# Performance work log

Measured on AMD Instinct MI355X. Metric: run time of the kernel, lower is better.

The kernel has to match this reference:

```python
import jax, jax.numpy as jnp
import numpy as np

D_MODEL = 1024
N_HEAD = 16
B, S = 4, 1024


def _linear(x, W, b):
    # torch nn.Linear: y = x @ W.T + b, W: [out, in]
    return jnp.einsum('bsd,ed->bse', x, W) + b


def _split(x):
    b, s, d = x.shape
    return x.reshape(b, s, N_HEAD, d // N_HEAD).transpose(0, 2, 1, 3)  # [b,h,s,dh]


def _concat(x):
    b, h, s, dh = x.shape
    return x.transpose(0, 2, 1, 3).reshape(b, s, h * dh)


def _attention(q, k, v):
    dh = q.shape[-1]
    scale = 1.0 / np.float32(np.sqrt(dh))
    scores = jnp.einsum('bhqd,bhkd->bhqk', q, k) * scale
    probs = jax.nn.softmax(scores, axis=-1)
    return jnp.einsum('bhqk,bhkd->bhqd', probs, v)


def setup_inputs() -> dict:
    key = jax.random.key(0)
    ks = jax.random.split(key, 20)
    sc = 1.0 / np.float32(np.sqrt(D_MODEL))
    inp = {
        'q': jax.random.normal(ks[0], (B, S, D_MODEL), jnp.float32),
        'k': jax.random.normal(ks[1], (B, S, D_MODEL), jnp.float32),
        'v': jax.random.normal(ks[2], (B, S, D_MODEL), jnp.float32),
    }
    names = ['Wq', 'Wk', 'Wv', 'Wq2', 'Wk2', 'Wv2', 'Wc', 'Wc2']
    for i, n in enumerate(names):
        inp[n] = jax.random.normal(ks[3 + i], (D_MODEL, D_MODEL), jnp.float32) * sc
        inp['b' + n[1:]] = jnp.zeros((D_MODEL,), jnp.float32)
    return inp


def reference(q, k, v, Wq, bq, Wk, bk, Wv, bv, Wq2, bq2, Wk2, bk2, Wv2, bv2, Wc, bc, Wc2, bc2):
    # path 1 projections
    q1 = _linear(q, Wq, bq)
    k1 = _linear(k, Wk, bk)
    v1 = _linear(v, Wv, bv)
    # path 2 projections (note cross-wiring: q2 from k, k2/v2 from q)
    q2 = _linear(k, Wq2, bq2)
    k2 = _linear(q, Wk2, bk2)
    v2 = _linear(q, Wv2, bv2)

    out1 = _attention(_split(q1), _split(k1), _split(v1))
    out2 = _attention(_split(q2), _split(k2), _split(v2))

    out1 = _linear(_concat(out1), Wc, bc)
    out2 = _linear(_concat(out2), Wc2, bc2)
    return out1, out2
```

## Files before the change

### kernel.cpp

```cpp
#include <hip/hip_runtime.h>
#include <hip/hip_bf16.h>

#define B_ 4
#define S_ 1024
#define D_ 1024
#define H_ 16
#define M_ 4096

typedef unsigned short u16;
typedef __attribute__((ext_vector_type(4))) float f32x4;
typedef __attribute__((ext_vector_type(16))) float f32x16;
typedef __attribute__((ext_vector_type(8))) short short8;
typedef __attribute__((ext_vector_type(4))) u16 u16x4;

__device__ inline u16 f2bf(float f) {
  return __builtin_bit_cast(u16, __float2bfloat16(f));
}

__device__ inline short8 ldfrag(const u16* p) {
  return *reinterpret_cast<const short8*>(p);
}

__device__ inline void gload_lds16(const void* g, void* l) {
  __builtin_amdgcn_global_load_lds((const __attribute__((address_space(1))) void*)g,
                                   (__attribute__((address_space(3))) void*)l,
                                   16, 0, 0);
}

__device__ inline int sigma_s(int s) {
  return (s & ~12) | ((s & 4) << 1) | ((s & 8) >> 1);
}

struct GArgs {
  const void* A[6];
  const void* W[6];
  const float* bias[6];
  void* C[6];
  float oscale[6];
  int vtrans[6];
};

struct CvtArgs {
  const float* src[11];
  u16* dst[11];
  int n4[11];
};

__global__ __launch_bounds__(256) void cvt_f32_bf16(CvtArgs a) {
  const int z = blockIdx.y;
  const float4* s = (const float4*)a.src[z];
  u16x4* d = (u16x4*)a.dst[z];
  const int n4 = a.n4[z];
  for (int i = blockIdx.x * blockDim.x + threadIdx.x; i < n4; i += gridDim.x * blockDim.x) {
    float4 v = s[i];
    u16x4 o;
    o[0] = f2bf(v.x); o[1] = f2bf(v.y); o[2] = f2bf(v.z); o[3] = f2bf(v.w);
    d[i] = o;
  }
}

template<typename CT>
__global__ __launch_bounds__(256) void gemm_bt_lds(GArgs args) {
  const int z = blockIdx.z;
  const u16* A = (const u16*)args.A[z];
  const u16* W = (const u16*)args.W[z];
  const float* bias = args.bias[z];
  CT* C = (CT*)args.C[z];
  const float oscale = args.oscale[z];
  const int vtrans = args.vtrans[z];

  __shared__ u16 Al[128 * 64];
  __shared__ u16 Bl[128 * 64];

  const int tid = threadIdx.x;
  const int lane = tid & 63;
  const int w = tid >> 6;
  const int wr = w >> 1, wc = w & 1;
  const int l15 = lane & 15, lhi = lane >> 4;

  const int lin = blockIdx.x + blockIdx.y * 8;
  const int xcd = lin & 7, idx = lin >> 3;
  const int bx = (xcd & 1) * 4 + (idx >> 3);
  const int by = (xcd >> 1) * 8 + (idx & 7);
  const int m0 = by * 128, n0 = bx * 128;

  const int srow = lane >> 3;
  const int scol = (lane & 7) * 8;

  const f32x4 vzero = {0.f, 0.f, 0.f, 0.f};
  f32x4 acc[4][4];
#pragma unroll
  for (int i = 0; i < 4; ++i)
#pragma unroll
    for (int j = 0; j < 4; ++j) acc[i][j] = vzero;

  for (int kt = 0; kt < 1024; kt += 64) {
    __syncthreads();
    const u16* Ag = A + (size_t)m0 * 1024 + kt;
    const u16* Wg = W + (size_t)n0 * 1024 + kt;
#pragma unroll
    for (int j = 0; j < 4; ++j) {
      int rb = w * 32 + j * 8;
      gload_lds16(Ag + (size_t)(rb + srow) * 1024 + scol, &Al[rb * 64]);
      gload_lds16(Wg + (size_t)(rb + srow) * 1024 + scol, &Bl[rb * 64]);
    }
    __syncthreads();

#pragma unroll
    for (int c = 0; c < 2; ++c) {
      short8 af[4], bfr[4];
#pragma unroll
      for (int i = 0; i < 4; ++i) af[i] = ldfrag(&Al[(wr * 64 + i * 16 + l15) * 64 + c * 32 + lhi * 8]);
#pragma unroll
      for (int j = 0; j < 4; ++j) bfr[j] = ldfrag(&Bl[(wc * 64 + j * 16 + l15) * 64 + c * 32 + lhi * 8]);
#pragma unroll
      for (int i = 0; i < 4; ++i)
#pragma unroll
        for (int j = 0; j < 4; ++j)
          acc[i][j] = __builtin_amdgcn_mfma_f32_16x16x32_bf16(af[i], bfr[j], acc[i][j], 0, 0, 0);
    }
  }

#pragma unroll
  for (int i = 0; i < 4; ++i) {
#pragma unroll
    for (int j = 0; j < 4; ++j) {
      int n = n0 + wc * 64 + j * 16 + l15;
      float bsv = bias[n];
      int mb = m0 + wr * 64 + i * 16 + lhi * 4;
      if (vtrans) {
        int h = n >> 6, d = n & 63;
        int b = mb >> 10, s0 = sigma_s(mb & 1023);
        u16x4 ov;
#pragma unroll
        for (int r = 0; r < 4; ++r) ov[r] = f2bf((acc[i][j][r] + bsv) * oscale);
        *reinterpret_cast<u16x4*>((u16*)C + ((size_t)((b * 16 + h) * 64 + d)) * 1024 + s0) = ov;
      } else {
#pragma unroll
        for (int r = 0; r < 4; ++r) {
          float val = (acc[i][j][r] + bsv) * oscale;
          if constexpr (sizeof(CT) == 2) ((u16*)C)[(size_t)(mb + r) * 1024 + n] = f2bf(val);
          else ((float*)C)[(size_t)(mb + r) * 1024 + n] = val;
        }
      }
    }
  }
}

template<typename AT, typename CT>
__global__ __launch_bounds__(256) void gemm_bt_batched(GArgs args) {
  const int z = blockIdx.z;
  const AT* A = (const AT*)args.A[z];
  const float* W = (const float*)args.W[z];
  const float* bias = args.bias[z];
  CT* C = (CT*)args.C[z];
  const float oscale = args.oscale[z];
  const int vtrans = args.vtrans[z];

  __shared__ u16 Al[128][72];
  __shared__ u16 Bl[128][72];

  const int tid = threadIdx.x;
  const int lane = tid & 63;
  const int wid = tid >> 6;
  const int wr = wid >> 1, wc = wid & 1;
  const int m0 = blockIdx.y * 128, n0 = blockIdx.x * 128;
  const int l15 = lane & 15, lhi = lane >> 4;

  const f32x4 vzero = {0.f, 0.f, 0.f, 0.f};
  f32x4 acc[4][4];
#pragma unroll
  for (int i = 0; i < 4; ++i)
#pragma unroll
    for (int j = 0; j < 4; ++j) acc[i][j] = vzero;

  for (int kt = 0; kt < 1024; kt += 64) {
    __syncthreads();
#pragma unroll
    for (int i = 0; i < 8; ++i) {
      int g = tid + i * 256;
      int row = g >> 4, col = (g & 15) * 4;
      u16x4 bv;
      if constexpr (sizeof(AT) == 4) {
        float4 vv = *reinterpret_cast<const float4*>((const float*)A + (size_t)(m0 + row) * 1024 + kt + col);
        bv[0] = f2bf(vv.x); bv[1] = f2bf(vv.y); bv[2] = f2bf(vv.z); bv[3] = f2bf(vv.w);
      } else {
        bv = *reinterpret_cast<const u16x4*>((const u16*)A + (size_t)(m0 + row) * 1024 + kt + col);
      }
      *reinterpret_cast<u16x4*>(&Al[row][col]) = bv;
    }
#pragma unroll
    for (int i = 0; i < 8; ++i) {
      int g = tid + i * 256;
      int row = g >> 4, col = (g & 15) * 4;
      float4 vv = *reinterpret_cast<const float4*>((const float*)W + (size_t)(n0 + row) * 1024 + kt + col);
      u16x4 bv;
      bv[0] = f2bf(vv.x); bv[1] = f2bf(vv.y); bv[2] = f2bf(vv.z); bv[3] = f2bf(vv.w);
      *reinterpret_cast<u16x4*>(&Bl[row][col]) = bv;
    }
    __syncthreads();

#pragma unroll
    for (int c = 0; c < 2; ++c) {
      short8 af[4], bfr[4];
#pragma unroll
      for (int i = 0; i < 4; ++i) af[i] = ldfrag(&Al[wr * 64 + i * 16 + l15][c * 32 + lhi * 8]);
#pragma unroll
      for (int j = 0; j < 4; ++j) bfr[j] = ldfrag(&Bl[wc * 64 + j * 16 + l15][c * 32 + lhi * 8]);
#pragma unroll
      for (int i = 0; i < 4; ++i)
#pragma unroll
        for (int j = 0; j < 4; ++j)
          acc[i][j] = __builtin_amdgcn_mfma_f32_16x16x32_bf16(af[i], bfr[j], acc[i][j], 0, 0, 0);
    }
  }

#pragma unroll
  for (int i = 0; i < 4; ++i) {
#pragma unroll
    for (int j = 0; j < 4; ++j) {
      int n = n0 + wc * 64 + j * 16 + l15;
      float bsv = bias[n];
      int mb = m0 + wr * 64 + i * 16 + lhi * 4;
      if (vtrans) {
        int h = n >> 6, d = n & 63;
        int b = mb >> 10, s0 = sigma_s(mb & 1023);
        u16x4 ov;
#pragma unroll
        for (int r = 0; r < 4; ++r) ov[r] = f2bf((acc[i][j][r] + bsv) * oscale);
        *reinterpret_cast<u16x4*>((u16*)C + ((size_t)((b * 16 + h) * 64 + d)) * 1024 + s0) = ov;
      } else {
#pragma unroll
        for (int r = 0; r < 4; ++r) {
          float val = (acc[i][j][r] + bsv) * oscale;
          if constexpr (sizeof(CT) == 2) ((u16*)C)[(size_t)(mb + r) * 1024 + n] = f2bf(val);
          else ((float*)C)[(size_t)(mb + r) * 1024 + n] = val;
        }
      }
    }
  }
}

__global__ __launch_bounds__(256, 2) void attn_fused32b(const u16* q1b, const u16* k1b, const u16* vt1,
                                                        const u16* q2b, const u16* k2b, const u16* vt2,
                                                        u16* o1, u16* o2) {
  const int qt = blockIdx.x;
  const int h = blockIdx.y;
  const int zb = blockIdx.z;
  const int path = zb >> 2, b = zb & 3;

  const u16* Q = (path == 0) ? q1b : q2b;
  const u16* K = (path == 0) ? k1b : k2b;
  const u16* V = (path == 0) ? vt1 : vt2;
  u16* O = (path == 0) ? o1 : o2;

  const size_t base_qk = (size_t)b * S_ * D_ + (size_t)h * 64;
  const size_t vbase = (size_t)((b * 16 + h) * 64) * 1024;
  const int tid = threadIdx.x;
  const int lane = tid & 63, w = tid >> 6;
  const int lq = lane & 31, hi = lane >> 5;

  __shared__ u16 Ks[2][64][72];
  __shared__ u16 Vs[2][64][72];

  const int srow = tid >> 3;
  const int scol = (tid & 7) * 8;

  const int qbase_row = qt * 256 + w * 64;
  short8 qf[2][4];
#pragma unroll
  for (int qtile = 0; qtile < 2; ++qtile)
#pragma unroll
    for (int dhg = 0; dhg < 4; ++dhg)
      qf[qtile][dhg] = ldfrag(Q + base_qk + (size_t)(qbase_row + qtile * 32 + lq) * 1024 + dhg * 16 + hi * 8);

  f32x16 o_acc[2][2] = {};
  float m_r[2] = {-1e30f, -1e30f};
  float l_r[2] = {0.f, 0.f};

  {
    short8 r0 = ldfrag(K + base_qk + (size_t)srow * 1024 + scol);
    short8 r1 = ldfrag(K + base_qk + (size_t)(srow + 32) * 1024 + scol);
    short8 r2 = ldfrag(V + vbase + (size_t)srow * 1024 + scol);
    short8 r3 = ldfrag(V + vbase + (size_t)(srow + 32) * 1024 + scol);
    *reinterpret_cast<short8*>(&Ks[0][srow][scol]) = r0;
    *reinterpret_cast<short8*>(&Ks[0][srow + 32][scol]) = r1;
    *reinterpret_cast<short8*>(&Vs[0][srow][scol]) = r2;
    *reinterpret_cast<short8*>(&Vs[0][srow + 32][scol]) = r3;
  }
  __syncthreads();

  for (int kv = 0; kv < 16; ++kv) {
    const int cur = kv & 1;

    short8 n0, n1, n2, n3;
    if (kv < 15) {
      const u16* kg = K + base_qk + (size_t)((kv + 1) * 64) * 1024;
      const u16* vg = V + vbase + (kv + 1) * 64;
      n0 = ldfrag(kg + (size_t)srow * 1024 + scol);
      n1 = ldfrag(kg + (size_t)(srow + 32) * 1024 + scol);
      n2 = ldfrag(vg + (size_t)srow * 1024 + scol);
      n3 = ldfrag(vg + (size_t)(srow + 32) * 1024 + scol);
    }

    f32x16 s[2][2] = {};
    __builtin_amdgcn_s_setprio(1);
#pragma unroll
    for (int dhg = 0; dhg < 4; ++dhg) {
#pragma unroll
      for (int keytile = 0; keytile < 2; ++keytile) {
        short8 ka = ldfrag(&Ks[cur][keytile * 32 + lq][dhg * 16 + hi * 8]);
#pragma unroll
        for (int qtile = 0; qtile < 2; ++qtile)
          s[keytile][qtile] = __builtin_amdgcn_mfma_f32_32x32x16_bf16(ka, qf[qtile][dhg], s[keytile][qtile], 0, 0, 0);
      }
    }
    __builtin_amdgcn_s_setprio(0);

#pragma unroll
    for (int qtile = 0; qtile < 2; ++qtile) {
      float pm = s[0][qtile][0];
#pragma unroll
      for (int r = 1; r < 16; ++r) pm = fmaxf(pm, s[0][qtile][r]);
#pragma unroll
      for (int r = 0; r < 16; ++r) pm = fmaxf(pm, s[1][qtile][r]);
      pm = fmaxf(pm, __shfl_xor(pm, 32));
      float mn = fmaxf(m_r[qtile], pm);
      float sc = __expf(m_r[qtile] - mn);
      m_r[qtile] = mn;
      float sum = 0.f;
#pragma unroll
      for (int kt = 0; kt < 2; ++kt)
#pragma unroll
        for (int r = 0; r < 16; ++r) {
          float e = __expf(s[kt][qtile][r] - mn);
          s[kt][qtile][r] = e;
          sum += e;
        }
      sum += __shfl_xor(sum, 32);
      l_r[qtile] = l_r[qtile] * sc + sum;
      o_acc[0][qtile] *= sc;
      o_acc[1][qtile] *= sc;
    }

    __builtin_amdgcn_s_setprio(1);
#pragma unroll
    for (int g = 0; g < 4; ++g) {
      short8 va0 = ldfrag(&Vs[cur][lq][g * 16 + hi * 8]);
      short8 va1 = ldfrag(&Vs[cur][32 + lq][g * 16 + hi * 8]);
#pragma unroll
      for (int qtile = 0; qtile < 2; ++qtile) {
        short8 pb;
#pragma unroll
        for (int j = 0; j < 8; ++j) {
          float pv = (g < 2) ? s[0][qtile][(g & 1) * 8 + j] : s[1][qtile][(g & 1) * 8 + j];
          pb[j] = (short)f2bf(pv);
        }
        o_acc[0][qtile] = __builtin_amdgcn_mfma_f32_32x32x16_bf16(va0, pb, o_acc[0][qtile], 0, 0, 0);
        o_acc[1][qtile] = __builtin_amdgcn_mfma_f32_32x32x16_bf16(va1, pb, o_acc[1][qtile], 0, 0, 0);
      }
    }
    __builtin_amdgcn_s_setprio(0);

    __syncthreads();
    if (kv < 15) {
      const int nxt = cur ^ 1;
      *reinterpret_cast<short8*>(&Ks[nxt][srow][scol]) = n0;
      *reinterpret_cast<short8*>(&Ks[nxt][srow + 32][scol]) = n1;
      *reinterpret_cast<short8*>(&Vs[nxt][srow][scol]) = n2;
      *reinterpret_cast<short8*>(&Vs[nxt][srow + 32][scol]) = n3;
      __syncthreads();
    }
  }

#pragma unroll
  for (int qtile = 0; qtile < 2; ++qtile) {
    float inv = 1.0f / l_r[qtile];
    u16* Op = O + base_qk + (size_t)(qbase_row + qtile * 32 + lq) * 1024;
#pragma unroll
    for (int dtile = 0; dtile < 2; ++dtile) {
#pragma unroll
      for (int qd = 0; qd < 4; ++qd) {
        u16x4 ov;
#pragma unroll
        for (int r = 0; r < 4; ++r) ov[r] = f2bf(o_acc[dtile][qtile][qd * 4 + r] * inv);
        *reinterpret_cast<u16x4*>(Op + dtile * 32 + 8 * qd + 4 * hi) = ov;
      }
    }
  }
}

extern "C" void kernel_launch(void* const* d_in, const int* in_sizes, int n_in,
                              void* d_out, int out_size, void* d_ws, size_t ws_size,
                              hipStream_t stream) {
  const float* q   = (const float*)d_in[0];
  const float* k   = (const float*)d_in[1];
  const float* v   = (const float*)d_in[2];
  const float* Wq  = (const float*)d_in[3];  const float* bq  = (const float*)d_in[4];
  const float* Wk  = (const float*)d_in[5];  const float* bk  = (const float*)d_in[6];
  const float* Wv  = (const float*)d_in[7];  const float* bv  = (const float*)d_in[8];
  const float* Wq2 = (const float*)d_in[9];  const float* bq2 = (const float*)d_in[10];
  const float* Wk2 = (const float*)d_in[11]; const float* bk2 = (const float*)d_in[12];
  const float* Wv2 = (const float*)d_in[13]; const float* bv2 = (const float*)d_in[14];
  const float* Wc  = (const float*)d_in[15]; const float* bc  = (const float*)d_in[16];
  const float* Wc2 = (const float*)d_in[17]; const float* bc2 = (const float*)d_in[18];

  u16* ws = (u16*)d_ws;
  const size_t SZ = (size_t)M_ * D_;
  const size_t WSZ = (size_t)D_ * D_;
  u16* q1b = ws + 0 * SZ;
  u16* k1b = ws + 1 * SZ;
  u16* vt1 = ws + 2 * SZ;
  u16* q2b = ws + 3 * SZ;
  u16* k2b = ws + 4 * SZ;
  u16* vt2 = ws + 5 * SZ;
  u16* a1  = ws + 6 * SZ;
  u16* a2  = ws + 7 * SZ;

  const size_t need = (11 * SZ + 8 * WSZ) * sizeof(u16);

  if (ws_size >= need) {
    u16* qb = ws + 8 * SZ;
    u16* kb = ws + 9 * SZ;
    u16* vb = ws + 10 * SZ;
    u16* wbase = ws + 11 * SZ;
    u16* WqB  = wbase + 0 * WSZ;
    u16* WkB  = wbase + 1 * WSZ;
    u16* WvB  = wbase + 2 * WSZ;
    u16* Wq2B = wbase + 3 * WSZ;
    u16* Wk2B = wbase + 4 * WSZ;
    u16* Wv2B = wbase + 5 * WSZ;
    u16* WcB  = wbase + 6 * WSZ;
    u16* Wc2B = wbase + 7 * WSZ;

    CvtArgs ca;
    ca.src[0] = q;   ca.dst[0] = qb;   ca.n4[0] = (int)(SZ / 4);
    ca.src[1] = k;   ca.dst[1] = kb;   ca.n4[1] = (int)(SZ / 4);
    ca.src[2] = v;   ca.dst[2] = vb;   ca.n4[2] = (int)(SZ / 4);
    ca.src[3] = Wq;  ca.dst[3] = WqB;  ca.n4[3] = (int)(WSZ / 4);
    ca.src[4] = Wk;  ca.dst[4] = WkB;  ca.n4[4] = (int)(WSZ / 4);
    ca.src[5] = Wv;  ca.dst[5] = WvB;  ca.n4[5] = (int)(WSZ / 4);
    ca.src[6] = Wq2; ca.dst[6] = Wq2B; ca.n4[6] = (int)(WSZ / 4);
    ca.src[7] = Wk2; ca.dst[7] = Wk2B; ca.n4[7] = (int)(WSZ / 4);
    ca.src[8] = Wv2; ca.dst[8] = Wv2B; ca.n4[8] = (int)(WSZ / 4);
    ca.src[9] = Wc;  ca.dst[9] = WcB;  ca.n4[9] = (int)(WSZ / 4);
    ca.src[10] = Wc2; ca.dst[10] = Wc2B; ca.n4[10] = (int)(WSZ / 4);
    cvt_f32_bf16<<<dim3(512, 11), dim3(256), 0, stream>>>(ca);

    GArgs pa;
    pa.A[0] = qb; pa.W[0] = WqB;  pa.bias[0] = bq;  pa.C[0] = q1b; pa.oscale[0] = 0.125f; pa.vtrans[0] = 0;
    pa.A[1] = kb; pa.W[1] = WkB;  pa.bias[1] = bk;  pa.C[1] = k1b; pa.oscale[1] = 1.0f;   pa.vtrans[1] = 0;
    pa.A[2] = vb; pa.W[2] = WvB;  pa.bias[2] = bv;  pa.C[2] = vt1; pa.oscale[2] = 1.0f;   pa.vtrans[2] = 1;
    pa.A[3] = kb; pa.W[3] = Wq2B; pa.bias[3] = bq2; pa.C[3] = q2b; pa.oscale[3] = 0.125f; pa.vtrans[3] = 0;
    pa.A[4] = qb; pa.W[4] = Wk2B; pa.bias[4] = bk2; pa.C[4] = k2b; pa.oscale[4] = 1.0f;   pa.vtrans[4] = 0;
    pa.A[5] = qb; pa.W[5] = Wv2B; pa.bias[5] = bv2; pa.C[5] = vt2; pa.oscale[5] = 1.0f;   pa.vtrans[5] = 1;
    gemm_bt_lds<u16><<<dim3(8, 32, 6), dim3(256), 0, stream>>>(pa);

    attn_fused32b<<<dim3(4, 16, 8), dim3(256), 0, stream>>>(q1b, k1b, vt1, q2b, k2b, vt2, a1, a2);

    GArgs fa;
    fa.A[0] = a1; fa.W[0] = WcB;  fa.bias[0] = bc;  fa.C[0] = (float*)d_out;      fa.oscale[0] = 1.0f; fa.vtrans[0] = 0;
    fa.A[1] = a2; fa.W[1] = Wc2B; fa.bias[1] = bc2; fa.C[1] = (float*)d_out + SZ; fa.oscale[1] = 1.0f; fa.vtrans[1] = 0;
    gemm_bt_lds<float><<<dim3(8, 32, 2), dim3(256), 0, stream>>>(fa);
  } else {
    GArgs pa;
    pa.A[0] = q; pa.W[0] = Wq;  pa.bias[0] = bq;  pa.C[0] = q1b; pa.oscale[0] = 0.125f; pa.vtrans[0] = 0;
    pa.A[1] = k; pa.W[1] = Wk;  pa.bias[1] = bk;  pa.C[1] = k1b; pa.oscale[1] = 1.0f;   pa.vtrans[1] = 0;
    pa.A[2] = v; pa.W[2] = Wv;  pa.bias[2] = bv;  pa.C[2] = vt1; pa.oscale[2] = 1.0f;   pa.vtrans[2] = 1;
    pa.A[3] = k; pa.W[3] = Wq2; pa.bias[3] = bq2; pa.C[3] = q2b; pa.oscale[3] = 0.125f; pa.vtrans[3] = 0;
    pa.A[4] = q; pa.W[4] = Wk2; pa.bias[4] = bk2; pa.C[4] = k2b; pa.oscale[4] = 1.0f;   pa.vtrans[4] = 0;
    pa.A[5] = q; pa.W[5] = Wv2; pa.bias[5] = bv2; pa.C[5] = vt2; pa.oscale[5] = 1.0f;   pa.vtrans[5] = 1;
    gemm_bt_batched<float, u16><<<dim3(8, 32, 6), dim3(256), 0, stream>>>(pa);

    attn_fused32b<<<dim3(4, 16, 8), dim3(256), 0, stream>>>(q1b, k1b, vt1, q2b, k2b, vt2, a1, a2);

    GArgs fa;
    fa.A[0] = a1; fa.W[0] = Wc;  fa.bias[0] = bc;  fa.C[0] = (float*)d_out;      fa.oscale[0] = 1.0f; fa.vtrans[0] = 0;
    fa.A[1] = a2; fa.W[1] = Wc2; fa.bias[1] = bc2; fa.C[1] = (float*)d_out + SZ; fa.oscale[1] = 1.0f; fa.vtrans[1] = 0;
    gemm_bt_batched<u16, float><<<dim3(8, 32, 2), dim3(256), 0, stream>>>(fa);
  }
}
```

Measured before the change: 185.3 us.

## Use 256x256-tile double-buffered GEMM for the six input projections

```diff
diff --git a/kernel.cpp b/kernel.cpp
--- a/kernel.cpp
+++ b/kernel.cpp
@@ -56,6 +56,112 @@
     u16x4 o;
     o[0] = f2bf(v.x); o[1] = f2bf(v.y); o[2] = f2bf(v.z); o[3] = f2bf(v.w);
     d[i] = o;
+  }
+}
+
+template<typename CT>
+__global__ __launch_bounds__(512, 2) void gemm_bt_256(GArgs args) {
+  const int z = blockIdx.z;
+  const u16* A = (const u16*)args.A[z];
+  const u16* W = (const u16*)args.W[z];
+  const float* bias = args.bias[z];
+  CT* C = (CT*)args.C[z];
+  const float oscale = args.oscale[z];
+  const int vtrans = args.vtrans[z];
+
+  __shared__ u16 AB[2][2][256 * 64];
+
+  const int tid = threadIdx.x;
+  const int lane = tid & 63;
+  const int w = tid >> 6;
+  const int wm = w >> 2, wn = w & 3;
+  const int l15 = lane & 15, lhi = lane >> 4;
+
+  const int lin = blockIdx.x + blockIdx.y * 4;
+  const int xcd = lin & 7, idx = lin >> 3;
+  const int by = xcd * 2 + (idx >> 2), bx = idx & 3;
+  const int m0 = by * 256, n0 = bx * 256;
+
+  const int srow = tid >> 3;
+  const int scol = (((tid & 7) ^ ((tid >> 3) & 7)) << 3);
+
+  f32x4 acc[8][4];
+#pragma unroll
+  for (int m = 0; m < 8; ++m)
+#pragma unroll
+    for (int n = 0; n < 4; ++n) acc[m][n] = f32x4{0.f, 0.f, 0.f, 0.f};
+
+  {
+    const u16* Ag = A + (size_t)m0 * 1024;
+    const u16* Wg = W + (size_t)n0 * 1024;
+#pragma unroll
+    for (int i = 0; i < 4; ++i) {
+      gload_lds16(Ag + (size_t)(i * 64 + srow) * 1024 + scol, &AB[0][0][i * 4096 + w * 512]);
+      gload_lds16(Wg + (size_t)(i * 64 + srow) * 1024 + scol, &AB[0][1][i * 4096 + w * 512]);
+    }
+  }
+  __syncthreads();
+
+  for (int t = 0; t < 16; ++t) {
+    const int db = t & 1;
+    if (t < 15) {
+      const u16* Ag = A + (size_t)m0 * 1024 + (t + 1) * 64;
+      const u16* Wg = W + (size_t)n0 * 1024 + (t + 1) * 64;
+#pragma unroll
+      for (int i = 0; i < 4; ++i) {
+        gload_lds16(Ag + (size_t)(i * 64 + srow) * 1024 + scol, &AB[db ^ 1][0][i * 4096 + w * 512]);
+        gload_lds16(Wg + (size_t)(i * 64 + srow) * 1024 + scol, &AB[db ^ 1][1][i * 4096 + w * 512]);
+      }
+    }
+
+#pragma unroll
+    for (int kk = 0; kk < 2; ++kk) {
+      short8 af[8], bf4[4];
+#pragma unroll
+      for (int m = 0; m < 8; ++m) {
+        int row = wm * 128 + m * 16 + l15;
+        af[m] = ldfrag(&AB[db][0][row * 64 + ((kk * 32 + lhi * 8) ^ ((l15 & 7) << 3))]);
+      }
+#pragma unroll
+      for (int n = 0; n < 4; ++n) {
+        int row = wn * 64 + n * 16 + l15;
+        bf4[n] = ldfrag(&AB[db][1][row * 64 + ((kk * 32 + lhi * 8) ^ ((l15 & 7) << 3))]);
+      }
+      __builtin_amdgcn_s_setprio(1);
+#pragma unroll
+      for (int m = 0; m < 8; ++m)
+#pragma unroll
+        for (int n = 0; n < 4; ++n)
+          acc[m][n] = __builtin_amdgcn_mfma_f32_16x16x32_bf16(af[m], bf4[n], acc[m][n], 0, 0, 0);
+      __builtin_amdgcn_s_setprio(0);
+    }
+
+    __syncthreads();
+  }
+
+#pragma unroll
+  for (int m = 0; m < 8; ++m) {
+#pragma unroll
+    for (int n = 0; n < 4; ++n) {
+      int ncol = n0 + wn * 64 + n * 16 + l15;
+      float bsv = bias[ncol];
+      int mb = m0 + wm * 128 + m * 16 + lhi * 4;
+      if (vtrans) {
+        int h = ncol >> 6, d = ncol & 63;
+        int b = mb >> 10, s0 = sigma_s(mb & 1023);
+        u16x4 ov;
+#pragma unroll
+        for (int r = 0; r < 4; ++r) ov[r] = f2bf((acc[m][n][r] + bsv) * oscale);
+        *reinterpret_cast<u16x4*>((u16*)C + ((size_t)((b * 16 + h) * 64 + d)) * 1024 + s0) = ov;
+      } else {
+#pragma unroll
+        for (int r = 0; r < 4; ++r) {
+          float val = (acc[m][n][r] + bsv) * oscale;
+          if constexpr (sizeof(CT) == 2) ((u16*)C)[(size_t)(mb + r) * 1024 + ncol] = f2bf(val);
+          else ((float*)C)[(size_t)(mb + r) * 1024 + ncol] = val;
+        }
+      }
+    }
   }
 }
 
@@ -454,7 +560,7 @@
     pa.A[3] = kb; pa.W[3] = Wq2B; pa.bias[3] = bq2; pa.C[3] = q2b; pa.oscale[3] = 0.125f; pa.vtrans[3] = 0;
     pa.A[4] = qb; pa.W[4] = Wk2B; pa.bias[4] = bk2; pa.C[4] = k2b; pa.oscale[4] = 1.0f;   pa.vtrans[4] = 0;
     pa.A[5] = qb; pa.W[5] = Wv2B; pa.bias[5] = bv2; pa.C[5] = vt2; pa.oscale[5] = 1.0f;   pa.vtrans[5] = 1;
-    gemm_bt_lds<u16><<<dim3(8, 32, 6), dim3(256), 0, stream>>>(pa);
+    gemm_bt_256<u16><<<dim3(4, 16, 6), dim3(512), 0, stream>>>(pa);
 
     attn_fused32b<<<dim3(4, 16, 8), dim3(256), 0, stream>>>(q1b, k1b, vt1, q2b, k2b, vt2, a1, a2);
 
```

Result: faster. 169.2 us (-8.7%).

## Replace bf16 GEMM with templated 4-stage pipelined K32 kernel with swizzled LDS

Applied to the files above, without the earlier changes.

```diff
diff --git a/kernel.cpp b/kernel.cpp
--- a/kernel.cpp
+++ b/kernel.cpp
@@ -59,8 +59,13 @@
   }
 }
 
-template<typename CT>
-__global__ __launch_bounds__(256) void gemm_bt_lds(GArgs args) {
+template<int MW, int NW, int MF, int NF, typename CT>
+__global__ __launch_bounds__(MW * NW * 64, 2) void gemm_k32(GArgs args) {
+  constexpr int T = MW * NW * 64;
+  constexpr int BM = MW * MF * 16;
+  constexpr int BN = NW * NF * 16;
+  constexpr int RPI = T / 4;
+
   const int z = blockIdx.z;
   const u16* A = (const u16*)args.A[z];
   const u16* W = (const u16*)args.W[z];
@@ -69,78 +74,100 @@
   const float oscale = args.oscale[z];
   const int vtrans = args.vtrans[z];
 
-  __shared__ u16 Al[128 * 64];
-  __shared__ u16 Bl[128 * 64];
+  __shared__ u16 LA[4][BM * 32];
+  __shared__ u16 LB[4][BN * 32];
 
   const int tid = threadIdx.x;
   const int lane = tid & 63;
   const int w = tid >> 6;
-  const int wr = w >> 1, wc = w & 1;
+  const int wm = w / NW, wn = w % NW;
   const int l15 = lane & 15, lhi = lane >> 4;
 
-  const int lin = blockIdx.x + blockIdx.y * 8;
-  const int xcd = lin & 7, idx = lin >> 3;
-  const int bx = (xcd & 1) * 4 + (idx >> 3);
-  const int by = (xcd >> 1) * 8 + (idx & 7);
-  const int m0 = by * 128, n0 = bx * 128;
-
-  const int srow = lane >> 3;
-  const int scol = (lane & 7) * 8;
-
-  const f32x4 vzero = {0.f, 0.f, 0.f, 0.f};
-  f32x4 acc[4][4];
-#pragma unroll
-  for (int i = 0; i < 4; ++i)
-#pragma unroll
-    for (int j = 0; j < 4; ++j) acc[i][j] = vzero;
-
-  for (int kt = 0; kt < 1024; kt += 64) {
-    __syncthreads();
-    const u16* Ag = A + (size_t)m0 * 1024 + kt;
-    const u16* Wg = W + (size_t)n0 * 1024 + kt;
-#pragma unroll
-    for (int j = 0; j < 4; ++j) {
-      int rb = w * 32 + j * 8;
-      gload_lds16(Ag + (size_t)(rb + srow) * 1024 + scol, &Al[rb * 64]);
-      gload_lds16(Wg + (size_t)(rb + srow) * 1024 + scol, &Bl[rb * 64]);
-    }
-    __syncthreads();
-
-#pragma unroll
-    for (int c = 0; c < 2; ++c) {
-      short8 af[4], bfr[4];
-#pragma unroll
-      for (int i = 0; i < 4; ++i) af[i] = ldfrag(&Al[(wr * 64 + i * 16 + l15) * 64 + c * 32 + lhi * 8]);
-#pragma unroll
-      for (int j = 0; j < 4; ++j) bfr[j] = ldfrag(&Bl[(wc * 64 + j * 16 + l15) * 64 + c * 32 + lhi * 8]);
-#pragma unroll
-      for (int i = 0; i < 4; ++i)
-#pragma unroll
-        for (int j = 0; j < 4; ++j)
-          acc[i][j] = __builtin_amdgcn_mfma_f32_16x16x32_bf16(af[i], bfr[j], acc[i][j], 0, 0, 0);
-    }
-  }
-
-#pragma unroll
-  for (int i = 0; i < 4; ++i) {
-#pragma unroll
-    for (int j = 0; j < 4; ++j) {
-      int n = n0 + wc * 64 + j * 16 + l15;
-      float bsv = bias[n];
-      int mb = m0 + wr * 64 + i * 16 + lhi * 4;
+  const int nwg = gridDim.x * gridDim.y;
+  const int lin = blockIdx.x + blockIdx.y * gridDim.x;
+  const int swz = (lin & 7) * (nwg >> 3) + (lin >> 3);
+  const int bx = swz % gridDim.x, by = swz / gridDim.x;
+  const int m0 = by * BM, n0 = bx * BN;
+
+  const int srow = tid >> 2;
+  const int sgcol = (((tid & 3) ^ (srow & 3)) << 3);
+
+  f32x4 acc[MF][NF];
+#pragma unroll
+  for (int m = 0; m < MF; ++m)
+#pragma unroll
+    for (int n = 0; n < NF; ++n) acc[m][n] = f32x4{0.f, 0.f, 0.f, 0.f};
+
+  const u16* Abase = A + (size_t)m0 * 1024;
+  const u16* Wbase = W + (size_t)n0 * 1024;
+
+  auto stage = [&](int ktile, int r) {
+    const u16* Ag = Abase + ktile * 32;
+    const u16* Wg = Wbase + ktile * 32;
+#pragma unroll
+    for (int i = 0; i < BM / RPI; ++i)
+      gload_lds16(Ag + (size_t)(i * RPI + srow) * 1024 + sgcol, &LA[r][i * RPI * 32 + w * 512]);
+#pragma unroll
+    for (int i = 0; i < BN / RPI; ++i)
+      gload_lds16(Wg + (size_t)(i * RPI + srow) * 1024 + sgcol, &LB[r][i * RPI * 32 + w * 512]);
+  };
+
+  stage(0, 0);
+  stage(1, 1);
+  stage(2, 2);
+  asm volatile("s_waitcnt vmcnt(8)" ::: "memory");
+  __builtin_amdgcn_s_barrier();
+  __builtin_amdgcn_sched_barrier(0);
+
+  for (int t = 0; t < 32; ++t) {
+    const int kp = (t + 3 < 32) ? t + 3 : 31;
+    stage(kp, (t + 3) & 3);
+
+    const int r = t & 3;
+    short8 af[MF], bf[NF];
+#pragma unroll
+    for (int m = 0; m < MF; ++m) {
+      int row = wm * (MF * 16) + m * 16 + l15;
+      af[m] = ldfrag(&LA[r][row * 32 + ((lhi ^ (row & 3)) << 3)]);
+    }
+#pragma unroll
+    for (int n = 0; n < NF; ++n) {
+      int row = wn * (NF * 16) + n * 16 + l15;
+      bf[n] = ldfrag(&LB[r][row * 32 + ((lhi ^ (row & 3)) << 3)]);
+    }
+    __builtin_amdgcn_s_setprio(1);
+#pragma unroll
+    for (int m = 0; m < MF; ++m)
+#pragma unroll
+      for (int n = 0; n < NF; ++n)
+        acc[m][n] = __builtin_amdgcn_mfma_f32_16x16x32_bf16(af[m], bf[n], acc[m][n], 0, 0, 0);
+    __builtin_amdgcn_s_setprio(0);
+
+    asm volatile("s_waitcnt vmcnt(8)" ::: "memory");
+    __builtin_amdgcn_s_barrier();
+    __builtin_amdgcn_sched_barrier(0);
+  }
+
+#pragma unroll
+  for (int m = 0; m < MF; ++m) {
+#pragma unroll
+    for (int n = 0; n < NF; ++n) {
+      int ncol = n0 + wn * (NF * 16) + n * 16 + l15;
+      float bsv = bias[ncol];
+      int mb = m0 + wm * (MF * 16) + m * 16 + lhi * 4;
       if (vtrans) {
-        int h = n >> 6, d = n & 63;
+        int h = ncol >> 6, d = ncol & 63;
         int b = mb >> 10, s0 = sigma_s(mb & 1023);
         u16x4 ov;
 #pragma unroll
-        for (int r = 0; r < 4; ++r) ov[r] = f2bf((acc[i][j][r] + bsv) * oscale);
+        for (int r2 = 0; r2 < 4; ++r2) ov[r2] = f2bf((acc[m][n][r2] + bsv) * oscale);
         *reinterpret_cast<u16x4*>((u16*)C + ((size_t)((b * 16 + h) * 64 + d)) * 1024 + s0) = ov;
       } else {
 #pragma unroll
-        for (int r = 0; r < 4; ++r) {
-          float val = (acc[i][j][r] + bsv) * oscale;
-          if constexpr (sizeof(CT) == 2) ((u16*)C)[(size_t)(mb + r) * 1024 + n] = f2bf(val);
-          else ((float*)C)[(size_t)(mb + r) * 1024 + n] = val;
+        for (int r2 = 0; r2 < 4; ++r2) {
+          float val = (acc[m][n][r2] + bsv) * oscale;
+          if constexpr (sizeof(CT) == 2) ((u16*)C)[(size_t)(mb + r2) * 1024 + ncol] = f2bf(val);
+          else ((float*)C)[(size_t)(mb + r2) * 1024 + ncol] = val;
         }
       }
     }
@@ -454,14 +481,14 @@
     pa.A[3] = kb; pa.W[3] = Wq2B; pa.bias[3] = bq2; pa.C[3] = q2b; pa.oscale[3] = 0.125f; pa.vtrans[3] = 0;
     pa.A[4] = qb; pa.W[4] = Wk2B; pa.bias[4] = bk2; pa.C[4] = k2b; pa.oscale[4] = 1.0f;   pa.vtrans[4] = 0;
     pa.A[5] = qb; pa.W[5] = Wv2B; pa.bias[5] = bv2; pa.C[5] = vt2; pa.oscale[5] = 1.0f;   pa.vtrans[5] = 1;
-    gemm_bt_lds<u16><<<dim3(8, 32, 6), dim3(256), 0, stream>>>(pa);
+    gemm_k32<2, 4, 8, 4, u16><<<dim3(4, 16, 6), dim3(512), 0, stream>>>(pa);
 
     attn_fused32b<<<dim3(4, 16, 8), dim3(256), 0, stream>>>(q1b, k1b, vt1, q2b, k2b, vt2, a1, a2);
 
     GArgs fa;
     fa.A[0] = a1; fa.W[0] = WcB;  fa.bias[0] = bc;  fa.C[0] = (float*)d_out;      fa.oscale[0] = 1.0f; fa.vtrans[0] = 0;
     fa.A[1] = a2; fa.W[1] = Wc2B; fa.bias[1] = bc2; fa.C[1] = (float*)d_out + SZ; fa.oscale[1] = 1.0f; fa.vtrans[1] = 0;
-    gemm_bt_lds<float><<<dim3(8, 32, 2), dim3(256), 0, stream>>>(fa);
+    gemm_k32<2, 2, 4, 4, float><<<dim3(8, 32, 2), dim3(256), 0, stream>>>(fa);
   } else {
     GArgs pa;
     pa.A[0] = q; pa.W[0] = Wq;  pa.bias[0] = bq;  pa.C[0] = q1b; pa.oscale[0] = 0.125f; pa.vtrans[0] = 0;
```

After: 198.8 us. 7.3% more time.
